# Kernel tuning notes

Hardware: AMD Instinct MI355X
Metric: run time of the kernel (lower is better)

## Reference

```python
import jax, jax.numpy as jnp
import numpy as np

N, S, E, H = 8, 1024, 1024, 16
DK = E // H


def setup_inputs() -> dict:
    key = jax.random.key(0)
    ks = jax.random.split(key, 12)
    scale = 1.0 / np.sqrt(E)
    inp = {
        "q": jax.random.normal(ks[0], (N, S, E), jnp.float32),
        "k": jax.random.normal(ks[1], (N, S, E), jnp.float32),
        "v": jax.random.normal(ks[2], (N, S, E), jnp.float32),
        "attn_mask": jax.random.randint(ks[3], (N, S, S), 0, 2).astype(bool),
        "wq": jax.random.normal(ks[4], (E, E), jnp.float32) * scale,
        "bq": jnp.zeros((E,), jnp.float32),
        "wk": jax.random.normal(ks[5], (E, E), jnp.float32) * scale,
        "bk": jnp.zeros((E,), jnp.float32),
        "wv": jax.random.normal(ks[6], (E, E), jnp.float32) * scale,
        "bv": jnp.zeros((E,), jnp.float32),
        "wo": jax.random.normal(ks[7], (E, E), jnp.float32) * scale,
        "bo": jnp.zeros((E,), jnp.float32),
    }
    return inp


def reference(q, k, v, attn_mask, wq, bq, wk, bk, wv, bv, wo, bo):
    # Linear projections (weights stored as (E_in, E_out)), split into heads.
    qh = (q @ wq + bq).reshape(N, S, H, DK).transpose(0, 2, 1, 3)  # (N,H,S,DK)
    kh = (k @ wk + bk).reshape(N, S, H, DK).transpose(0, 2, 1, 3)
    vh = (v @ wv + bv).reshape(N, S, H, DK).transpose(0, 2, 1, 3)
    logits = jnp.einsum("nhsd,nhtd->nhst", qh, kh) / np.sqrt(DK)  # (N,H,S,S)
    eps = 1e9
    logits = jnp.where(attn_mask[:, None, :, :], -eps, logits)
    attn_weights = jax.nn.softmax(logits, axis=-1)
    # dropout layers are identity in eval mode
    o = jnp.einsum("nhst,nhtd->nhsd", attn_weights, vh)  # (N,H,S,DK)
    o = o.transpose(0, 2, 1, 3).reshape(N, S, E)
    o = o @ wo + bo
    return o, attn_weights
```

## Files before the change

### kernel.cpp

```cpp
#include <hip/hip_runtime.h>
#include <cstdint>
#include <cstddef>

#define NB 8
#define SL 1024
#define ED 1024
#define NH 16
#define DKH 64

typedef __attribute__((ext_vector_type(4))) float f32x4;
typedef __attribute__((ext_vector_type(8))) short short8;

#define LDSW 40

__device__ __forceinline__ unsigned short bf16_rn(float x) {
    unsigned int u = __float_as_uint(x);
    u += 0x7FFFu + ((u >> 16) & 1u);
    return (unsigned short)(u >> 16);
}
__device__ __forceinline__ float bf16_f(unsigned short h) {
    return __uint_as_float(((unsigned int)h) << 16);
}
__device__ __forceinline__ void split2(float x, unsigned short& hi, unsigned short& lo) {
    unsigned short h = bf16_rn(x);
    hi = h;
    lo = bf16_rn(x - bf16_f(h));
}

template<bool APRE>
__device__ __forceinline__ void gemm_core2(
    const float* __restrict__ Af,
    const unsigned short* __restrict__ Ahg, const unsigned short* __restrict__ Alg,
    int lda,
    const unsigned short* __restrict__ Bhg, const unsigned short* __restrict__ Blg,
    int ldb,
    int Kd, int m0, int n0, f32x4 acc[4])
{
    __shared__ unsigned short Ahi[64 * LDSW];
    __shared__ unsigned short Alo[64 * LDSW];
    __shared__ unsigned short Bhi[64 * LDSW];
    __shared__ unsigned short Blo[64 * LDSW];

    const int tid  = threadIdx.x;
    const int wave = tid >> 6;
    const int lane = tid & 63;
    const int quad = lane >> 4;
    const int l16  = lane & 15;
    const int r    = tid >> 2;
    const int cc   = (tid & 3) * 8;

#pragma unroll
    for (int j = 0; j < 4; j++) acc[j] = (f32x4)(0.0f);

    for (int k0 = 0; k0 < Kd; k0 += 32) {
        __syncthreads();
        if constexpr (APRE) {
            const size_t off = (size_t)(m0 + r) * lda + k0 + cc;
            *(short8*)&Ahi[r * LDSW + cc] = *(const short8*)(Ahg + off);
            *(short8*)&Alo[r * LDSW + cc] = *(const short8*)(Alg + off);
        } else {
            const float* p = Af + (size_t)(m0 + r) * lda + k0 + cc;
            const float4 v0 = *(const float4*)p;
            const float4 v1 = *(const float4*)(p + 4);
            short8 h8, l8;
            unsigned short h, l;
            split2(v0.x, h, l); h8[0] = (short)h; l8[0] = (short)l;
            split2(v0.y, h, l); h8[1] = (short)h; l8[1] = (short)l;
            split2(v0.z, h, l); h8[2] = (short)h; l8[2] = (short)l;
            split2(v0.w, h, l); h8[3] = (short)h; l8[3] = (short)l;
            split2(v1.x, h, l); h8[4] = (short)h; l8[4] = (short)l;
            split2(v1.y, h, l); h8[5] = (short)h; l8[5] = (short)l;
            split2(v1.z, h, l); h8[6] = (short)h; l8[6] = (short)l;
            split2(v1.w, h, l); h8[7] = (short)h; l8[7] = (short)l;
            *(short8*)&Ahi[r * LDSW + cc] = h8;
            *(short8*)&Alo[r * LDSW + cc] = l8;
        }
        {
            const size_t off = (size_t)(n0 + r) * ldb + k0 + cc;
            *(short8*)&Bhi[r * LDSW + cc] = *(const short8*)(Bhg + off);
            *(short8*)&Blo[r * LDSW + cc] = *(const short8*)(Blg + off);
        }
        __syncthreads();

        const short8 ah = *(const short8*)&Ahi[(wave * 16 + l16) * LDSW + quad * 8];
        const short8 al = *(const short8*)&Alo[(wave * 16 + l16) * LDSW + quad * 8];
#pragma unroll
        for (int j = 0; j < 4; j++) {
            const short8 bh = *(const short8*)&Bhi[(j * 16 + l16) * LDSW + quad * 8];
            const short8 bl = *(const short8*)&Blo[(j * 16 + l16) * LDSW + quad * 8];
            acc[j] = __builtin_amdgcn_mfma_f32_16x16x32_bf16(al, bh, acc[j], 0, 0, 0);
            acc[j] = __builtin_amdgcn_mfma_f32_16x16x32_bf16(ah, bl, acc[j], 0, 0, 0);
            acc[j] = __builtin_amdgcn_mfma_f32_16x16x32_bf16(ah, bh, acc[j], 0, 0, 0);
        }
    }
}

__global__ __launch_bounds__(256)
void k_wsplitT(const float* __restrict__ W,
               unsigned short* __restrict__ Th, unsigned short* __restrict__ Tl)
{
    __shared__ float tile[64 * 65];
    const int n0 = blockIdx.x * 64;
    const int k0 = blockIdx.y * 64;
    const int tid = threadIdx.x;
    for (int i = tid; i < 64 * 64; i += 256) {
        const int rk = i >> 6, cn = i & 63;
        tile[rk * 65 + cn] = W[(size_t)(k0 + rk) * ED + n0 + cn];
    }
    __syncthreads();
    for (int i = tid; i < 64 * 64; i += 256) {
        const int rn = i >> 6, ck = i & 63;
        unsigned short h, l;
        split2(tile[ck * 65 + rn], h, l);
        Th[(size_t)(n0 + rn) * ED + k0 + ck] = h;
        Tl[(size_t)(n0 + rn) * ED + k0 + ck] = l;
    }
}

__global__ __launch_bounds__(256)
void k_projQK(const float* __restrict__ X,
              const unsigned short* __restrict__ Wh, const unsigned short* __restrict__ Wl,
              const float* __restrict__ bias,
              unsigned short* __restrict__ Oh, unsigned short* __restrict__ Ol)
{
    const int m0 = blockIdx.x * 64;
    const int n0 = blockIdx.y * 64;
    f32x4 acc[4];
    gemm_core2<false>(X, nullptr, nullptr, ED, Wh, Wl, ED, ED, m0, n0, acc);

    const int tid = threadIdx.x, wave = tid >> 6, lane = tid & 63;
    const int quad = lane >> 4, l16 = lane & 15;
#pragma unroll
    for (int j = 0; j < 4; j++) {
        const int col = n0 + j * 16 + l16;
        const int h = col >> 6, d = col & 63;
        const float b = bias[col];
#pragma unroll
        for (int rr = 0; rr < 4; rr++) {
            const int m = m0 + wave * 16 + quad * 4 + rr;
            const int n = m >> 10, s = m & 1023;
            const size_t idx = (((size_t)(n * NH + h)) * SL + s) * DKH + d;
            unsigned short hh, ll;
            split2(acc[j][rr] + b, hh, ll);
            Oh[idx] = hh;
            Ol[idx] = ll;
        }
    }
}

__global__ __launch_bounds__(256)
void k_projV(const float* __restrict__ X,
             const unsigned short* __restrict__ Wh, const unsigned short* __restrict__ Wl,
             const float* __restrict__ bias,
             unsigned short* __restrict__ Th, unsigned short* __restrict__ Tl)
{
    const int m0 = blockIdx.x * 64;
    const int n0 = blockIdx.y * 64;
    f32x4 acc[4];
    gemm_core2<false>(X, nullptr, nullptr, ED, Wh, Wl, ED, ED, m0, n0, acc);

    __shared__ unsigned int T[64 * 65];
    const int tid = threadIdx.x, wave = tid >> 6, lane = tid & 63;
    const int quad = lane >> 4, l16 = lane & 15;
#pragma unroll
    for (int j = 0; j < 4; j++) {
        const int d = j * 16 + l16;
        const float b = bias[n0 + d];
#pragma unroll
        for (int rr = 0; rr < 4; rr++) {
            const int sl = wave * 16 + quad * 4 + rr;
            unsigned short hh, ll;
            split2(acc[j][rr] + b, hh, ll);
            T[sl * 65 + d] = (unsigned int)hh | ((unsigned int)ll << 16);
        }
    }
    __syncthreads();
    const int d  = tid >> 2;
    const int sc = (tid & 3) * 16;
    const int ghead = (m0 >> 10) * NH + (n0 >> 6);
    const int sbase = (m0 & 1023) + sc;
    short8 h0, h1, l0, l1;
#pragma unroll
    for (int i = 0; i < 8; i++) {
        const unsigned int u = T[(sc + i) * 65 + d];
        h0[i] = (short)(u & 0xFFFFu);
        l0[i] = (short)(u >> 16);
    }
#pragma unroll
    for (int i = 0; i < 8; i++) {
        const unsigned int u = T[(sc + 8 + i) * 65 + d];
        h1[i] = (short)(u & 0xFFFFu);
        l1[i] = (short)(u >> 16);
    }
    const size_t off = ((size_t)ghead * DKH + d) * SL + sbase;
    *(short8*)(Th + off)     = h0;
    *(short8*)(Th + off + 8) = h1;
    *(short8*)(Tl + off)     = l0;
    *(short8*)(Tl + off + 8) = l1;
}

__global__ __launch_bounds__(256)
void k_logits(const unsigned short* __restrict__ qh_h, const unsigned short* __restrict__ qh_l,
              const unsigned short* __restrict__ kh_h, const unsigned short* __restrict__ kh_l,
              const int* __restrict__ mask, float* __restrict__ attn)
{
    const int head = blockIdx.z;
    const int n = head >> 4;
    const int m0 = blockIdx.x * 64;
    const int n0 = blockIdx.y * 64;
    const size_t hb = (size_t)head * SL * DKH;
    f32x4 acc[4];
    gemm_core2<true>(nullptr, qh_h + hb, qh_l + hb, DKH,
                     kh_h + hb, kh_l + hb, DKH, DKH, m0, n0, acc);

    const int tid = threadIdx.x, wave = tid >> 6, lane = tid & 63;
    const int quad = lane >> 4, l16 = lane & 15;
    const float scale = 0.125f;
#pragma unroll
    for (int j = 0; j < 4; j++) {
        const int t = n0 + j * 16 + l16;
#pragma unroll
        for (int rr = 0; rr < 4; rr++) {
            const int s = m0 + wave * 16 + quad * 4 + rr;
            float vv = acc[j][rr] * scale;
            if (mask[((size_t)n * SL + s) * SL + t]) vv = -1e9f;
            attn[((size_t)head * SL + s) * SL + t] = vv;
        }
    }
}

__global__ __launch_bounds__(256)
void k_softmax(float* __restrict__ attn)
{
    const int tid = threadIdx.x;
    const int wave = tid >> 6, lane = tid & 63;
    const size_t row = (size_t)blockIdx.x * 4 + wave;
    float* p = attn + row * SL;

    float4 v[4];
    float mx = -3.4e38f;
#pragma unroll
    for (int i = 0; i < 4; i++) {
        v[i] = *(const float4*)(p + lane * 4 + i * 256);
        mx = fmaxf(mx, fmaxf(fmaxf(v[i].x, v[i].y), fmaxf(v[i].z, v[i].w)));
    }
#pragma unroll
    for (int o = 32; o > 0; o >>= 1) mx = fmaxf(mx, __shfl_xor(mx, o));

    float sum = 0.0f;
#pragma unroll
    for (int i = 0; i < 4; i++) {
        v[i].x = __expf(v[i].x - mx);
        v[i].y = __expf(v[i].y - mx);
        v[i].z = __expf(v[i].z - mx);
        v[i].w = __expf(v[i].w - mx);
        sum += v[i].x + v[i].y + v[i].z + v[i].w;
    }
#pragma unroll
    for (int o = 32; o > 0; o >>= 1) sum += __shfl_xor(sum, o);

    const float inv = 1.0f / sum;
#pragma unroll
    for (int i = 0; i < 4; i++) {
        v[i].x *= inv; v[i].y *= inv; v[i].z *= inv; v[i].w *= inv;
        *(float4*)(p + lane * 4 + i * 256) = v[i];
    }
}

__global__ __launch_bounds__(256)
void k_pv(const float* __restrict__ attn,
          const unsigned short* __restrict__ vTh, const unsigned short* __restrict__ vTl,
          unsigned short* __restrict__ Oh, unsigned short* __restrict__ Ol)
{
    const int head = blockIdx.z;
    const int m0 = blockIdx.x * 64;
    const float* P = attn + (size_t)head * SL * SL;
    const unsigned short* Bh = vTh + (size_t)head * DKH * SL;
    const unsigned short* Bl = vTl + (size_t)head * DKH * SL;
    f32x4 acc[4];
    gemm_core2<false>(P, nullptr, nullptr, SL, Bh, Bl, SL, SL, m0, 0, acc);

    const int tid = threadIdx.x, wave = tid >> 6, lane = tid & 63;
    const int quad = lane >> 4, l16 = lane & 15;
    const int n = head >> 4, h = head & 15;
#pragma unroll
    for (int j = 0; j < 4; j++) {
        const int d = j * 16 + l16;
#pragma unroll
        for (int rr = 0; rr < 4; rr++) {
            const int s = m0 + wave * 16 + quad * 4 + rr;
            const size_t idx = ((size_t)n * SL + s) * ED + h * DKH + d;
            unsigned short hh, ll;
            split2(acc[j][rr], hh, ll);
            Oh[idx] = hh;
            Ol[idx] = ll;
        }
    }
}

__global__ __launch_bounds__(256)
void k_outproj(const unsigned short* __restrict__ Ah, const unsigned short* __restrict__ Al,
               const unsigned short* __restrict__ Wh, const unsigned short* __restrict__ Wl,
               const float* __restrict__ bias, float* __restrict__ out)
{
    const int m0 = blockIdx.x * 64;
    const int n0 = blockIdx.y * 64;
    f32x4 acc[4];
    gemm_core2<true>(nullptr, Ah, Al, ED, Wh, Wl, ED, ED, m0, n0, acc);

    const int tid = threadIdx.x, wave = tid >> 6, lane = tid & 63;
    const int quad = lane >> 4, l16 = lane & 15;
#pragma unroll
    for (int j = 0; j < 4; j++) {
        const int col = n0 + j * 16 + l16;
        const float b = bias[col];
#pragma unroll
        for (int rr = 0; rr < 4; rr++) {
            const int m = m0 + wave * 16 + quad * 4 + rr;
            out[(size_t)m * ED + col] = acc[j][rr] + b;
        }
    }
}

extern "C" void kernel_launch(void* const* d_in, const int* in_sizes, int n_in,
                              void* d_out, int out_size, void* d_ws, size_t ws_size,
                              hipStream_t stream) {
    const float* q    = (const float*)d_in[0];
    const float* k    = (const float*)d_in[1];
    const float* v    = (const float*)d_in[2];
    const int*   mask = (const int*)d_in[3];
    const float* wq = (const float*)d_in[4];
    const float* bq = (const float*)d_in[5];
    const float* wk = (const float*)d_in[6];
    const float* bk = (const float*)d_in[7];
    const float* wv = (const float*)d_in[8];
    const float* bv = (const float*)d_in[9];
    const float* wo = (const float*)d_in[10];
    const float* bo = (const float*)d_in[11];

    float* out  = (float*)d_out;
    float* attn = out + (size_t)NB * SL * ED;

    unsigned short* w = (unsigned short*)d_ws;
    const size_t WPL = (size_t)ED * ED;
    unsigned short* wqT_h = w + 0 * WPL;
    unsigned short* wqT_l = w + 1 * WPL;
    unsigned short* wkT_h = w + 2 * WPL;
    unsigned short* wkT_l = w + 3 * WPL;
    unsigned short* wvT_h = w + 4 * WPL;
    unsigned short* wvT_l = w + 5 * WPL;
    unsigned short* woT_h = w + 6 * WPL;
    unsigned short* woT_l = w + 7 * WPL;
    unsigned short* base  = w + 8 * WPL;
    const size_t HPL = (size_t)NB * NH * SL * DKH;
    unsigned short* qh_h = base + 0 * HPL;
    unsigned short* qh_l = base + 1 * HPL;
    unsigned short* kh_h = base + 2 * HPL;
    unsigned short* kh_l = base + 3 * HPL;
    unsigned short* vT_h = base + 4 * HPL;
    unsigned short* vT_l = base + 5 * HPL;
    unsigned short* oh_h = qh_h;
    unsigned short* oh_l = qh_l;

    const dim3 blk(256);
    const dim3 gw(ED / 64, ED / 64);
    hipLaunchKernelGGL(k_wsplitT, gw, blk, 0, stream, wq, wqT_h, wqT_l);
    hipLaunchKernelGGL(k_wsplitT, gw, blk, 0, stream, wk, wkT_h, wkT_l);
    hipLaunchKernelGGL(k_wsplitT, gw, blk, 0, stream, wv, wvT_h, wvT_l);
    hipLaunchKernelGGL(k_wsplitT, gw, blk, 0, stream, wo, woT_h, woT_l);

    const dim3 gproj(8192 / 64, ED / 64);
    hipLaunchKernelGGL(k_projQK, gproj, blk, 0, stream, q, wqT_h, wqT_l, bq, qh_h, qh_l);
    hipLaunchKernelGGL(k_projQK, gproj, blk, 0, stream, k, wkT_h, wkT_l, bk, kh_h, kh_l);
    hipLaunchKernelGGL(k_projV,  gproj, blk, 0, stream, v, wvT_h, wvT_l, bv, vT_h, vT_l);

    const dim3 glog(SL / 64, SL / 64, NB * NH);
    hipLaunchKernelGGL(k_logits, glog, blk, 0, stream, qh_h, qh_l, kh_h, kh_l, mask, attn);

    hipLaunchKernelGGL(k_softmax, dim3(NB * NH * SL / 4), blk, 0, stream, attn);

    hipLaunchKernelGGL(k_pv, dim3(SL / 64, 1, NB * NH), blk, 0, stream, attn, vT_h, vT_l, oh_h, oh_l);

    hipLaunchKernelGGL(k_outproj, gproj, blk, 0, stream, oh_h, oh_l, woT_h, woT_l, bo, out);
}
```

Measured before the change: 1.485 ms.

## Use larger double-buffered GEMM tiles with async global-to-LDS loads

Replaces the 64x64 single-buffered split-bf16 GEMM core with a templated core that uses 128x128 or 128x64 block tiles, several MFMA tiles per wave, double-buffered LDS, and global_load_lds DMA for the pre-split bf16 operands. The fp32 A operand is prefetched into registers while the current tile computes, and its LDS writes use an XOR swizzle. The aim is more reuse per byte loaded, fewer barriers per FLOP, and hiding global latency. In exchange it uses more LDS and registers, which lowers occupancy, and it launches fewer blocks for the smaller grids.

```diff
diff --git a/kernel.cpp b/kernel.cpp
--- a/kernel.cpp
+++ b/kernel.cpp
@@ -11,8 +11,6 @@
 typedef __attribute__((ext_vector_type(4))) float f32x4;
 typedef __attribute__((ext_vector_type(8))) short short8;
 
-#define LDSW 40
-
 __device__ __forceinline__ unsigned short bf16_rn(float x) {
     unsigned int u = __float_as_uint(x);
     u += 0x7FFFu + ((u >> 16) & 1u);
@@ -27,71 +25,150 @@
     lo = bf16_rn(x - bf16_f(h));
 }
 
-template<bool APRE>
-__device__ __forceinline__ void gemm_core2(
+__device__ __forceinline__ void dma16(const unsigned short* src, unsigned short* dst) {
+    __builtin_amdgcn_global_load_lds(
+        (const __attribute__((address_space(1))) void*)src,
+        (__attribute__((address_space(3))) void*)dst,
+        16, 0, 0);
+}
+
+template<int ROWS>
+__device__ __forceinline__ void dma_plane(
+    const unsigned short* __restrict__ g, unsigned short* l,
+    int ld, int r0, int k0, int wave, int lane)
+{
+    for (int i = wave; i < ROWS / 16; i += 4) {
+        const unsigned short* src =
+            g + (size_t)(r0 + i * 16 + (lane >> 2)) * ld + k0 + (lane & 3) * 8;
+        dma16(src, l + i * 512);
+    }
+}
+
+template<bool APRE, int BM, int BN, int WR, int WC, int ROWG, int COLT>
+__device__ __forceinline__ void gemm_core3(
+    unsigned short* smem,
     const float* __restrict__ Af,
     const unsigned short* __restrict__ Ahg, const unsigned short* __restrict__ Alg,
     int lda,
     const unsigned short* __restrict__ Bhg, const unsigned short* __restrict__ Blg,
-    int ldb,
-    int Kd, int m0, int n0, f32x4 acc[4])
-{
-    __shared__ unsigned short Ahi[64 * LDSW];
-    __shared__ unsigned short Alo[64 * LDSW];
-    __shared__ unsigned short Bhi[64 * LDSW];
-    __shared__ unsigned short Blo[64 * LDSW];
+    int ldb, int Kd, int m0, int n0,
+    f32x4 (&acc)[ROWG][COLT])
+{
+    static_assert(WR * WC == 4, "4 waves");
+    static_assert(16 * ROWG * WR == BM, "rows");
+    static_assert(16 * COLT * WC == BN, "cols");
+    static_assert(APRE || BM == 128, "fp32 staging assumes BM=128");
+
+    constexpr int ASZ = BM * 32;
+    constexpr int BSZ = BN * 32;
+    unsigned short* Ah = smem;
+    unsigned short* Al = smem + 2 * ASZ;
+    unsigned short* Bh = smem + 4 * ASZ;
+    unsigned short* Bl = smem + 4 * ASZ + 2 * BSZ;
 
     const int tid  = threadIdx.x;
     const int wave = tid >> 6;
     const int lane = tid & 63;
     const int quad = lane >> 4;
     const int l16  = lane & 15;
-    const int r    = tid >> 2;
-    const int cc   = (tid & 3) * 8;
-
-#pragma unroll
-    for (int j = 0; j < 4; j++) acc[j] = (f32x4)(0.0f);
-
-    for (int k0 = 0; k0 < Kd; k0 += 32) {
-        __syncthreads();
-        if constexpr (APRE) {
-            const size_t off = (size_t)(m0 + r) * lda + k0 + cc;
-            *(short8*)&Ahi[r * LDSW + cc] = *(const short8*)(Ahg + off);
-            *(short8*)&Alo[r * LDSW + cc] = *(const short8*)(Alg + off);
-        } else {
-            const float* p = Af + (size_t)(m0 + r) * lda + k0 + cc;
-            const float4 v0 = *(const float4*)p;
-            const float4 v1 = *(const float4*)(p + 4);
+    const int wr   = wave / WC;
+    const int wc   = wave % WC;
+
+#pragma unroll
+    for (int g = 0; g < ROWG; g++)
+#pragma unroll
+        for (int jt = 0; jt < COLT; jt++) acc[g][jt] = (f32x4)(0.0f);
+
+    const int ar  = tid >> 1;
+    const int acb = (tid & 1) * 2;
+
+    auto load_a = [&](int kk, float4 st[4]) {
+        const float* p = Af + (size_t)(m0 + ar) * lda + kk + (tid & 1) * 16;
+        st[0] = *(const float4*)(p + 0);
+        st[1] = *(const float4*)(p + 4);
+        st[2] = *(const float4*)(p + 8);
+        st[3] = *(const float4*)(p + 12);
+    };
+    auto write_a = [&](int b, const float4 st[4]) {
+        unsigned short* dh = Ah + b * ASZ;
+        unsigned short* dl = Al + b * ASZ;
+#pragma unroll
+        for (int w = 0; w < 2; w++) {
+            const int csw = (acb + w) ^ ((ar >> 1) & 3);
+            const float4 u0 = st[2 * w], u1 = st[2 * w + 1];
             short8 h8, l8;
             unsigned short h, l;
-            split2(v0.x, h, l); h8[0] = (short)h; l8[0] = (short)l;
-            split2(v0.y, h, l); h8[1] = (short)h; l8[1] = (short)l;
-            split2(v0.z, h, l); h8[2] = (short)h; l8[2] = (short)l;
-            split2(v0.w, h, l); h8[3] = (short)h; l8[3] = (short)l;
-            split2(v1.x, h, l); h8[4] = (short)h; l8[4] = (short)l;
-            split2(v1.y, h, l); h8[5] = (short)h; l8[5] = (short)l;
-            split2(v1.z, h, l); h8[6] = (short)h; l8[6] = (short)l;
-            split2(v1.w, h, l); h8[7] = (short)h; l8[7] = (short)l;
-            *(short8*)&Ahi[r * LDSW + cc] = h8;
-            *(short8*)&Alo[r * LDSW + cc] = l8;
-        }
-        {
-            const size_t off = (size_t)(n0 + r) * ldb + k0 + cc;
-            *(short8*)&Bhi[r * LDSW + cc] = *(const short8*)(Bhg + off);
-            *(short8*)&Blo[r * LDSW + cc] = *(const short8*)(Blg + off);
+            split2(u0.x, h, l); h8[0] = (short)h; l8[0] = (short)l;
+            split2(u0.y, h, l); h8[1] = (short)h; l8[1] = (short)l;
+            split2(u0.z, h, l); h8[2] = (short)h; l8[2] = (short)l;
+            split2(u0.w, h, l); h8[3] = (short)h; l8[3] = (short)l;
+            split2(u1.x, h, l); h8[4] = (short)h; l8[4] = (short)l;
+            split2(u1.y, h, l); h8[5] = (short)h; l8[5] = (short)l;
+            split2(u1.z, h, l); h8[6] = (short)h; l8[6] = (short)l;
+            split2(u1.w, h, l); h8[7] = (short)h; l8[7] = (short)l;
+            *(short8*)&dh[ar * 32 + csw * 8] = h8;
+            *(short8*)&dl[ar * 32 + csw * 8] = l8;
+        }
+    };
+    auto stage_b = [&](int b, int kk) {
+        dma_plane<BN>(Bhg, Bh + b * BSZ, ldb, n0, kk, wave, lane);
+        dma_plane<BN>(Blg, Bl + b * BSZ, ldb, n0, kk, wave, lane);
+    };
+    auto stage_a_dma = [&](int b, int kk) {
+        dma_plane<BM>(Ahg, Ah + b * ASZ, lda, m0, kk, wave, lane);
+        dma_plane<BM>(Alg, Al + b * ASZ, lda, m0, kk, wave, lane);
+    };
+
+    if constexpr (APRE) {
+        stage_a_dma(0, 0);
+    } else {
+        float4 st[4];
+        load_a(0, st);
+        write_a(0, st);
+    }
+    stage_b(0, 0);
+    __syncthreads();
+
+    int buf = 0;
+    for (int k0 = 0; k0 < Kd; k0 += 32) {
+        const int nk = k0 + 32;
+        float4 st[4];
+        if (nk < Kd) {
+            if constexpr (APRE) stage_a_dma(buf ^ 1, nk);
+            else                load_a(nk, st);
+            stage_b(buf ^ 1, nk);
+        }
+        const unsigned short* pAh = Ah + buf * ASZ;
+        const unsigned short* pAl = Al + buf * ASZ;
+        const unsigned short* pBh = Bh + buf * BSZ;
+        const unsigned short* pBl = Bl + buf * BSZ;
+        short8 ah[ROWG], al[ROWG];
+#pragma unroll
+        for (int g = 0; g < ROWG; g++) {
+            const int row = wr * (16 * ROWG) + g * 16 + l16;
+            int co;
+            if constexpr (APRE) co = quad * 8;
+            else                co = (quad ^ ((row >> 1) & 3)) * 8;
+            ah[g] = *(const short8*)&pAh[row * 32 + co];
+            al[g] = *(const short8*)&pAl[row * 32 + co];
+        }
+#pragma unroll
+        for (int jt = 0; jt < COLT; jt++) {
+            const int brow = wc * (16 * COLT) + jt * 16 + l16;
+            const short8 bh = *(const short8*)&pBh[brow * 32 + quad * 8];
+            const short8 bl = *(const short8*)&pBl[brow * 32 + quad * 8];
+#pragma unroll
+            for (int g = 0; g < ROWG; g++) {
+                acc[g][jt] = __builtin_amdgcn_mfma_f32_16x16x32_bf16(al[g], bh, acc[g][jt], 0, 0, 0);
+                acc[g][jt] = __builtin_amdgcn_mfma_f32_16x16x32_bf16(ah[g], bl, acc[g][jt], 0, 0, 0);
+                acc[g][jt] = __builtin_amdgcn_mfma_f32_16x16x32_bf16(ah[g], bh, acc[g][jt], 0, 0, 0);
+            }
+        }
+        if constexpr (!APRE) {
+            if (nk < Kd) write_a(buf ^ 1, st);
         }
         __syncthreads();
-
-        const short8 ah = *(const short8*)&Ahi[(wave * 16 + l16) * LDSW + quad * 8];
-        const short8 al = *(const short8*)&Alo[(wave * 16 + l16) * LDSW + quad * 8];
-#pragma unroll
-        for (int j = 0; j < 4; j++) {
-            const short8 bh = *(const short8*)&Bhi[(j * 16 + l16) * LDSW + quad * 8];
-            const short8 bl = *(const short8*)&Blo[(j * 16 + l16) * LDSW + quad * 8];
-            acc[j] = __builtin_amdgcn_mfma_f32_16x16x32_bf16(al, bh, acc[j], 0, 0, 0);
-            acc[j] = __builtin_amdgcn_mfma_f32_16x16x32_bf16(ah, bl, acc[j], 0, 0, 0);
-            acc[j] = __builtin_amdgcn_mfma_f32_16x16x32_bf16(ah, bh, acc[j], 0, 0, 0);
-        }
+        buf ^= 1;
     }
 }
 
@@ -123,27 +200,33 @@
               const float* __restrict__ bias,
               unsigned short* __restrict__ Oh, unsigned short* __restrict__ Ol)
 {
-    const int m0 = blockIdx.x * 64;
-    const int n0 = blockIdx.y * 64;
-    f32x4 acc[4];
-    gemm_core2<false>(X, nullptr, nullptr, ED, Wh, Wl, ED, ED, m0, n0, acc);
+    __shared__ unsigned short smem[(128 + 128) * 128];
+    const int m0 = blockIdx.x * 128;
+    const int n0 = blockIdx.y * 128;
+    f32x4 acc[4][4];
+    gemm_core3<false, 128, 128, 2, 2, 4, 4>(smem, X, nullptr, nullptr, ED,
+                                            Wh, Wl, ED, ED, m0, n0, acc);
 
     const int tid = threadIdx.x, wave = tid >> 6, lane = tid & 63;
     const int quad = lane >> 4, l16 = lane & 15;
-#pragma unroll
-    for (int j = 0; j < 4; j++) {
-        const int col = n0 + j * 16 + l16;
+    const int wr = wave >> 1, wc = wave & 1;
+#pragma unroll
+    for (int jt = 0; jt < 4; jt++) {
+        const int col = n0 + wc * 64 + jt * 16 + l16;
         const int h = col >> 6, d = col & 63;
         const float b = bias[col];
 #pragma unroll
-        for (int rr = 0; rr < 4; rr++) {
-            const int m = m0 + wave * 16 + quad * 4 + rr;
-            const int n = m >> 10, s = m & 1023;
-            const size_t idx = (((size_t)(n * NH + h)) * SL + s) * DKH + d;
-            unsigned short hh, ll;
-            split2(acc[j][rr] + b, hh, ll);
-            Oh[idx] = hh;
-            Ol[idx] = ll;
+        for (int g = 0; g < 4; g++) {
+#pragma unroll
+            for (int rr = 0; rr < 4; rr++) {
+                const int m = m0 + wr * 64 + g * 16 + quad * 4 + rr;
+                const int n = m >> 10, s = m & 1023;
+                const size_t idx = (((size_t)(n * NH + h)) * SL + s) * DKH + d;
+                unsigned short hh, ll;
+                split2(acc[g][jt][rr] + b, hh, ll);
+                Oh[idx] = hh;
+                Ol[idx] = ll;
+            }
         }
     }
 }
@@ -154,49 +237,48 @@
              const float* __restrict__ bias,
              unsigned short* __restrict__ Th, unsigned short* __restrict__ Tl)
 {
-    const int m0 = blockIdx.x * 64;
+    __shared__ unsigned short smem[(128 + 64) * 128];
+    const int m0 = blockIdx.x * 128;
     const int n0 = blockIdx.y * 64;
-    f32x4 acc[4];
-    gemm_core2<false>(X, nullptr, nullptr, ED, Wh, Wl, ED, ED, m0, n0, acc);
-
-    __shared__ unsigned int T[64 * 65];
+    f32x4 acc[2][4];
+    gemm_core3<false, 128, 64, 4, 1, 2, 4>(smem, X, nullptr, nullptr, ED,
+                                           Wh, Wl, ED, ED, m0, n0, acc);
+
+    unsigned int* T = (unsigned int*)smem;
     const int tid = threadIdx.x, wave = tid >> 6, lane = tid & 63;
     const int quad = lane >> 4, l16 = lane & 15;
 #pragma unroll
-    for (int j = 0; j < 4; j++) {
-        const int d = j * 16 + l16;
+    for (int jt = 0; jt < 4; jt++) {
+        const int d = jt * 16 + l16;
         const float b = bias[n0 + d];
 #pragma unroll
-        for (int rr = 0; rr < 4; rr++) {
-            const int sl = wave * 16 + quad * 4 + rr;
-            unsigned short hh, ll;
-            split2(acc[j][rr] + b, hh, ll);
-            T[sl * 65 + d] = (unsigned int)hh | ((unsigned int)ll << 16);
+        for (int g = 0; g < 2; g++) {
+#pragma unroll
+            for (int rr = 0; rr < 4; rr++) {
+                const int sl = wave * 32 + g * 16 + quad * 4 + rr;
+                unsigned short hh, ll;
+                split2(acc[g][jt][rr] + b, hh, ll);
+                T[sl * 65 + d] = (unsigned int)hh | ((unsigned int)ll << 16);
+            }
         }
     }
     __syncthreads();
     const int d  = tid >> 2;
-    const int sc = (tid & 3) * 16;
+    const int sc = (tid & 3) * 32;
     const int ghead = (m0 >> 10) * NH + (n0 >> 6);
-    const int sbase = (m0 & 1023) + sc;
-    short8 h0, h1, l0, l1;
-#pragma unroll
-    for (int i = 0; i < 8; i++) {
-        const unsigned int u = T[(sc + i) * 65 + d];
-        h0[i] = (short)(u & 0xFFFFu);
-        l0[i] = (short)(u >> 16);
-    }
-#pragma unroll
-    for (int i = 0; i < 8; i++) {
-        const unsigned int u = T[(sc + 8 + i) * 65 + d];
-        h1[i] = (short)(u & 0xFFFFu);
-        l1[i] = (short)(u >> 16);
-    }
-    const size_t off = ((size_t)ghead * DKH + d) * SL + sbase;
-    *(short8*)(Th + off)     = h0;
-    *(short8*)(Th + off + 8) = h1;
-    *(short8*)(Tl + off)     = l0;
-    *(short8*)(Tl + off + 8) = l1;
+    const size_t rowbase = ((size_t)ghead * DKH + d) * SL + (m0 & 1023) + sc;
+#pragma unroll
+    for (int c = 0; c < 4; c++) {
+        short8 h8, l8;
+#pragma unroll
+        for (int i = 0; i < 8; i++) {
+            const unsigned int u = T[(sc + c * 8 + i) * 65 + d];
+            h8[i] = (short)(u & 0xFFFFu);
+            l8[i] = (short)(u >> 16);
+        }
+        *(short8*)(Th + rowbase + c * 8) = h8;
+        *(short8*)(Tl + rowbase + c * 8) = l8;
+    }
 }
 
 __global__ __launch_bounds__(256)
@@ -204,27 +286,32 @@
               const unsigned short* __restrict__ kh_h, const unsigned short* __restrict__ kh_l,
               const int* __restrict__ mask, float* __restrict__ attn)
 {
+    __shared__ unsigned short smem[(128 + 128) * 128];
     const int head = blockIdx.z;
     const int n = head >> 4;
-    const int m0 = blockIdx.x * 64;
-    const int n0 = blockIdx.y * 64;
+    const int m0 = blockIdx.x * 128;
+    const int n0 = blockIdx.y * 128;
     const size_t hb = (size_t)head * SL * DKH;
-    f32x4 acc[4];
-    gemm_core2<true>(nullptr, qh_h + hb, qh_l + hb, DKH,
-                     kh_h + hb, kh_l + hb, DKH, DKH, m0, n0, acc);
+    f32x4 acc[4][4];
+    gemm_core3<true, 128, 128, 2, 2, 4, 4>(smem, nullptr, qh_h + hb, qh_l + hb, DKH,
+                                           kh_h + hb, kh_l + hb, DKH, DKH, m0, n0, acc);
 
     const int tid = threadIdx.x, wave = tid >> 6, lane = tid & 63;
     const int quad = lane >> 4, l16 = lane & 15;
+    const int wr = wave >> 1, wc = wave & 1;
     const float scale = 0.125f;
 #pragma unroll
-    for (int j = 0; j < 4; j++) {
-        const int t = n0 + j * 16 + l16;
-#pragma unroll
-        for (int rr = 0; rr < 4; rr++) {
-            const int s = m0 + wave * 16 + quad * 4 + rr;
-            float vv = acc[j][rr] * scale;
-            if (mask[((size_t)n * SL + s) * SL + t]) vv = -1e9f;
-            attn[((size_t)head * SL + s) * SL + t] = vv;
+    for (int jt = 0; jt < 4; jt++) {
+        const int t = n0 + wc * 64 + jt * 16 + l16;
+#pragma unroll
+        for (int g = 0; g < 4; g++) {
+#pragma unroll
+            for (int rr = 0; rr < 4; rr++) {
+                const int s = m0 + wr * 64 + g * 16 + quad * 4 + rr;
+                float vv = acc[g][jt][rr] * scale;
+                if (mask[((size_t)n * SL + s) * SL + t]) vv = -1e9f;
+                attn[((size_t)head * SL + s) * SL + t] = vv;
+            }
         }
     }
 }
@@ -272,28 +359,33 @@
           const unsigned short* __restrict__ vTh, const unsigned short* __restrict__ vTl,
           unsigned short* __restrict__ Oh, unsigned short* __restrict__ Ol)
 {
+    __shared__ unsigned short smem[(128 + 64) * 128];
     const int head = blockIdx.z;
-    const int m0 = blockIdx.x * 64;
+    const int m0 = blockIdx.x * 128;
     const float* P = attn + (size_t)head * SL * SL;
     const unsigned short* Bh = vTh + (size_t)head * DKH * SL;
     const unsigned short* Bl = vTl + (size_t)head * DKH * SL;
-    f32x4 acc[4];
-    gemm_core2<false>(P, nullptr, nullptr, SL, Bh, Bl, SL, SL, m0, 0, acc);
+    f32x4 acc[2][4];
+    gemm_core3<false, 128, 64, 4, 1, 2, 4>(smem, P, nullptr, nullptr, SL,
+                                           Bh, Bl, SL, SL, m0, 0, acc);
 
     const int tid = threadIdx.x, wave = tid >> 6, lane = tid & 63;
     const int quad = lane >> 4, l16 = lane & 15;
     const int n = head >> 4, h = head & 15;
 #pragma unroll
-    for (int j = 0; j < 4; j++) {
-        const int d = j * 16 + l16;
-#pragma unroll
-        for (int rr = 0; rr < 4; rr++) {
-            const int s = m0 + wave * 16 + quad * 4 + rr;
-            const size_t idx = ((size_t)n * SL + s) * ED + h * DKH + d;
-            unsigned short hh, ll;
-            split2(acc[j][rr], hh, ll);
-            Oh[idx] = hh;
-            Ol[idx] = ll;
+    for (int jt = 0; jt < 4; jt++) {
+        const int d = jt * 16 + l16;
+#pragma unroll
+        for (int g = 0; g < 2; g++) {
+#pragma unroll
+            for (int rr = 0; rr < 4; rr++) {
+                const int s = m0 + wave * 32 + g * 16 + quad * 4 + rr;
+                const size_t idx = ((size_t)n * SL + s) * ED + h * DKH + d;
+                unsigned short hh, ll;
+                split2(acc[g][jt][rr], hh, ll);
+                Oh[idx] = hh;
+                Ol[idx] = ll;
+            }
         }
     }
 }
@@ -303,21 +395,27 @@
                const unsigned short* __restrict__ Wh, const unsigned short* __restrict__ Wl,
                const float* __restrict__ bias, float* __restrict__ out)
 {
-    const int m0 = blockIdx.x * 64;
-    const int n0 = blockIdx.y * 64;
-    f32x4 acc[4];
-    gemm_core2<true>(nullptr, Ah, Al, ED, Wh, Wl, ED, ED, m0, n0, acc);
+    __shared__ unsigned short smem[(128 + 128) * 128];
+    const int m0 = blockIdx.x * 128;
+    const int n0 = blockIdx.y * 128;
+    f32x4 acc[4][4];
+    gemm_core3<true, 128, 128, 2, 2, 4, 4>(smem, nullptr, Ah, Al, ED,
+                                           Wh, Wl, ED, ED, m0, n0, acc);
 
     const int tid = threadIdx.x, wave = tid >> 6, lane = tid & 63;
     const int quad = lane >> 4, l16 = lane & 15;
-#pragma unroll
-    for (int j = 0; j < 4; j++) {
-        const int col = n0 + j * 16 + l16;
+    const int wr = wave >> 1, wc = wave & 1;
+#pragma unroll
+    for (int jt = 0; jt < 4; jt++) {
+        const int col = n0 + wc * 64 + jt * 16 + l16;
         const float b = bias[col];
 #pragma unroll
-        for (int rr = 0; rr < 4; rr++) {
-            const int m = m0 + wave * 16 + quad * 4 + rr;
-            out[(size_t)m * ED + col] = acc[j][rr] + b;
+        for (int g = 0; g < 4; g++) {
+#pragma unroll
+            for (int rr = 0; rr < 4; rr++) {
+                const int m = m0 + wr * 64 + g * 16 + quad * 4 + rr;
+                out[(size_t)m * ED + col] = acc[g][jt][rr] + b;
+            }
         }
     }
 }
@@ -369,17 +467,20 @@
     hipLaunchKernelGGL(k_wsplitT, gw, blk, 0, stream, wv, wvT_h, wvT_l);
     hipLaunchKernelGGL(k_wsplitT, gw, blk, 0, stream, wo, woT_h, woT_l);
 
-    const dim3 gproj(8192 / 64, ED / 64);
+    const dim3 gproj(8192 / 128, ED / 128);
     hipLaunchKernelGGL(k_projQK, gproj, blk, 0, stream, q, wqT_h, wqT_l, bq, qh_h, qh_l);
     hipLaunchKernelGGL(k_projQK, gproj, blk, 0, stream, k, wkT_h, wkT_l, bk, kh_h, kh_l);
-    hipLaunchKernelGGL(k_projV,  gproj, blk, 0, stream, v, wvT_h, wvT_l, bv, vT_h, vT_l);
-
-    const dim3 glog(SL / 64, SL / 64, NB * NH);
+
+    const dim3 gprojV(8192 / 128, ED / 64);
+    hipLaunchKernelGGL(k_projV, gprojV, blk, 0, stream, v, wvT_h, wvT_l, bv, vT_h, vT_l);
+
+    const dim3 glog(SL / 128, SL / 128, NB * NH);
     hipLaunchKernelGGL(k_logits, glog, blk, 0, stream, qh_h, qh_l, kh_h, kh_l, mask, attn);
 
     hipLaunchKernelGGL(k_softmax, dim3(NB * NH * SL / 4), blk, 0, stream, attn);
 
-    hipLaunchKernelGGL(k_pv, dim3(SL / 64, 1, NB * NH), blk, 0, stream, attn, vT_h, vT_l, oh_h, oh_l);
+    const dim3 gpv(SL / 128, 1, NB * NH);
+    hipLaunchKernelGGL(k_pv, gpv, blk, 0, stream, attn, vT_h, vT_l, oh_h, oh_l);
 
     hipLaunchKernelGGL(k_outproj, gproj, blk, 0, stream, oh_h, oh_l, woT_h, woT_l, bo, out);
 }
```

New measurement: 1.495 ms. Within noise of the previous version (+0.7%).
